# Kernel optimization log

Measured on AMD Instinct MI355X. Metric: run time of the kernel, lower is better.

Reference implementation:

```python
import jax, jax.numpy as jnp
import numpy as np

N_QUERY, N_BACKGND, DIM = 2048, 8192, 32


def setup_inputs() -> dict:
    key = jax.random.key(0)
    k0, k1, k2, k3 = jax.random.split(key, 4)
    x_backgnd = jax.random.normal(k0, (N_BACKGND, DIM), dtype=jnp.float32)
    y_backgnd = jax.random.normal(k1, (N_BACKGND,), dtype=jnp.float32)
    x_query = jax.random.normal(k2, (N_QUERY, DIM), dtype=jnp.float32)
    r = jax.random.uniform(k3, (N_QUERY, N_BACKGND), dtype=jnp.float32)
    sigma = jnp.array([0.1], dtype=jnp.float32)      # nn.Parameter init_sigma
    r_scale = jnp.array([3.0], dtype=jnp.float32)    # nn.Parameter init_r_scale
    w = jnp.ones((DIM,), dtype=jnp.float32)          # trainable weights matrix
    return {"x_backgnd": x_backgnd, "y_backgnd": y_backgnd, "x_query": x_query,
            "r": r, "sigma": sigma, "r_scale": r_scale, "w": w}


def reference(x_backgnd, y_backgnd, x_query, r, sigma, r_scale, w):
    # weighted Euclidean distance: ||(xq - xb) * w|| via the expansion trick,
    # avoiding the (n_query, n_backgnd, dim) difference tensor.
    xq = x_query * w           # (nq, d)
    xb = x_backgnd * w         # (nb, d)
    q2 = jnp.sum(xq * xq, axis=1, keepdims=True)        # (nq, 1)
    b2 = jnp.sum(xb * xb, axis=1)                        # (nb,)
    d2 = q2 + b2[None, :] - 2.0 * (xq @ xb.T)            # (nq, nb)
    dists = jnp.sqrt(jnp.maximum(d2, 0.0))
    # exp kernel with relationship bias, normalize, weighted sum
    k_vals = jnp.exp(-dists / sigma + r_scale * r)       # sigma, r_scale broadcast (1,)
    k_sum = jnp.sum(k_vals, axis=1, keepdims=True) + 1e-8
    weights = k_vals / k_sum
    y_pred = weights @ y_backgnd                          # (nq,)
    return y_pred
```

## Files before the change

kernel.cpp:

```cpp
#include <hip/hip_runtime.h>
#include <math.h>

#define NQ 2048
#define NB 8192
#define DIM 32

#define LOG2E 1.44269504088896340736f

typedef _Float16 half8 __attribute__((ext_vector_type(8)));
typedef float    f32x4 __attribute__((ext_vector_type(4)));

#define WS_ACC 0
#define WS_Q2  16448
#define WS_B2  24640
#define WS_XQH 57408
#define WS_XBH 188480

__global__ __launch_bounds__(256) void relnw_pre(
    const float* __restrict__ xq, const float* __restrict__ xb,
    const float* __restrict__ w,
    _Float16* __restrict__ XQh, _Float16* __restrict__ XBh,
    float* __restrict__ q2, float* __restrict__ b2,
    float* __restrict__ acc)
{
    const int tid = threadIdx.x;
    const int gi  = blockIdx.x * 256 + tid;
    if (gi < 2 * NQ) acc[gi] = 0.f;

    const int row = blockIdx.x * 64 + (tid >> 2);
    const int p   = tid & 3;
    if (row >= NQ + NB) return;

    const float* src; _Float16* dst; float* s2; float scale;
    if (row < NQ) { src = xq + (size_t)row * DIM;
                    dst = XQh + (size_t)row * DIM; s2 = q2 + row; scale = 1.f; }
    else          { int j = row - NQ;
                    src = xb + (size_t)j * DIM;
                    dst = XBh + (size_t)j * DIM;   s2 = b2 + j;   scale = -2.f; }

    const float4 xa  = ((const float4*)src)[p * 2];
    const float4 xbv = ((const float4*)src)[p * 2 + 1];
    const float4 wa  = ((const float4*)w)[p * 2];
    const float4 wb  = ((const float4*)w)[p * 2 + 1];
    const float xs[8]  = {xa.x, xa.y, xa.z, xa.w, xbv.x, xbv.y, xbv.z, xbv.w};
    const float ws_[8] = {wa.x, wa.y, wa.z, wa.w, wb.x, wb.y, wb.z, wb.w};

    half8 h;
    float s = 0.f;
#pragma unroll
    for (int c = 0; c < 8; ++c) {
        float t = xs[c] * ws_[c];
        _Float16 hh = (_Float16)t;
        float th = (float)hh;
        s = fmaf(th, th, s);
        h[c] = (_Float16)(th * scale);
    }
    *(half8*)(dst + p * 8) = h;

    s += __shfl_xor(s, 1, 64);
    s += __shfl_xor(s, 2, 64);
    if (p == 0) *s2 = s;
}

#define BT_PER_WAVE 16
#define BG_PER_WAVE (BT_PER_WAVE * 16)

#define GLDS(GSRC, LDST)                                                    \
  __builtin_amdgcn_global_load_lds(                                         \
      (const __attribute__((address_space(1))) void*)(GSRC),                \
      (__attribute__((address_space(3))) void*)(LDST), 16, 0, 0)

#define SBAR __builtin_amdgcn_sched_barrier(0)

#define COMPQ(BUF, QTR, AF)                                                 \
  { _Pragma("unroll") for (int it = 0; it < 4; ++it) {                      \
      const int co = (QTR) * 64 + it * 16 + quad * 4;                       \
      const f32x4 bb = *(const f32x4*)(b2l + co);                           \
      const f32x4 yv = *(const f32x4*)(ybl + co);                           \
      const f32x4 rr = *(const f32x4*)((BUF) + m * 256 +                    \
                           ((it * 64 + quad * 16) ^ swz));                  \
      f32x4 cin;                                                            \
      _Pragma("unroll") for (int g = 0; g < 4; ++g) cin[g] = q2s + bb[g];   \
      const f32x4 d2v = __builtin_amdgcn_mfma_f32_16x16x32_f16(             \
          AF[it], qfrag, cin, 0, 0, 0);                                     \
      _Pragma("unroll") for (int g = 0; g < 4; ++g) {                       \
        float d2   = fmaxf(d2v[g], 0.f);                                    \
        float dist = __builtin_amdgcn_sqrtf(d2);                            \
        float e    = fmaf(dist, c1, rr[g] * c2);                            \
        float k    = __builtin_amdgcn_exp2f(e);                             \
        sk += k;                                                            \
        sky = fmaf(k, yv[g], sky); } } }

__global__ __launch_bounds__(256, 2) void relnw_main(
    const _Float16* __restrict__ XQh,
    const _Float16* __restrict__ XBh,
    const float* __restrict__ q2,
    const float* __restrict__ b2,
    const float* __restrict__ yb,
    const float* __restrict__ r,
    const float* __restrict__ sigma,
    const float* __restrict__ rscale,
    float* __restrict__ acc)
{
    __shared__ char lds[4 * 8192 + 4 * 1024 + 4 * 1024];

    const int tid  = threadIdx.x;
    const int lane = tid & 63;
    const int wid  = tid >> 6;
    const int m    = lane & 15;
    const int quad = lane >> 4;

    const int q0     = blockIdx.y * 16;
    const int bstart = (blockIdx.x * 4 + wid) * BG_PER_WAVE;

    char*  bufA = lds + wid * 8192;
    char*  bufB = bufA + 4096;
    float* b2l  = (float*)(lds + 32768 + wid * 1024);
    float* ybl  = (float*)(lds + 36864 + wid * 1024);

    const float c1 = -LOG2E / sigma[0];
    const float c2 =  LOG2E * rscale[0];

    const half8 qfrag = *(const half8*)(XQh + (size_t)(q0 + m) * DIM + quad * 8);
    const float q2s   = q2[q0 + m];
    const int   swz   = (m & 7) << 4;

    const int g16 = lane >> 4;
    const int l16 = lane & 15;
    const char* rsrc[4];
#pragma unroll
    for (int j = 0; j < 4; ++j) {
        const int rw = 4 * j + g16;
        rsrc[j] = (const char*)(r + (size_t)(q0 + rw) * NB + bstart)
                  + ((l16 * 16) ^ ((rw & 7) << 4));
    }

#define AFRAG(I) (*(const half8*)(XBh + \
        (size_t)(bstart + (I) * 16 + m) * DIM + quad * 8))

    half8 afA[4], afB[4], afC[4], afD[4];
    float sk = 0.f, sky = 0.f;

#pragma unroll
    for (int i = 0; i < 4; ++i) afA[i] = AFRAG(i);
#pragma unroll
    for (int i = 0; i < 4; ++i) afB[i] = AFRAG(4 + i);
    GLDS((const char*)(b2 + bstart) + lane * 16, b2l);
    GLDS((const char*)(yb + bstart) + lane * 16, ybl);
#pragma unroll
    for (int j = 0; j < 4; ++j) GLDS(rsrc[j],       bufA + j * 1024);
#pragma unroll
    for (int j = 0; j < 4; ++j) GLDS(rsrc[j] + 256, bufB + j * 1024);
    SBAR;
    asm volatile("s_waitcnt vmcnt(4)" ::: "memory");
    SBAR;

    COMPQ(bufA, 0, afA)

#pragma unroll
    for (int i = 0; i < 4; ++i) afC[i] = AFRAG(8 + i);
#pragma unroll
    for (int i = 0; i < 4; ++i) afD[i] = AFRAG(12 + i);
#pragma unroll
    for (int j = 0; j < 4; ++j) GLDS(rsrc[j] + 512, bufA + j * 1024);
    SBAR;
    asm volatile("s_waitcnt vmcnt(12)" ::: "memory");
    SBAR;

    COMPQ(bufB, 1, afB)

#pragma unroll
    for (int j = 0; j < 4; ++j) GLDS(rsrc[j] + 768, bufB + j * 1024);
    SBAR;
    asm volatile("s_waitcnt vmcnt(4)" ::: "memory");
    SBAR;

    COMPQ(bufA, 2, afC)

    asm volatile("s_waitcnt vmcnt(0)" ::: "memory");
    SBAR;

    COMPQ(bufB, 3, afD)

    sk  += __shfl_xor(sk, 16, 64);
    sk  += __shfl_xor(sk, 32, 64);
    sky += __shfl_xor(sky, 16, 64);
    sky += __shfl_xor(sky, 32, 64);
    if (lane < 16) {
        atomicAdd(acc + (q0 + m),      sk);
        atomicAdd(acc + NQ + (q0 + m), sky);
    }
}

__global__ __launch_bounds__(256) void relnw_finalize(
    const float* __restrict__ acc, float* __restrict__ out)
{
    int q = blockIdx.x * 256 + threadIdx.x;
    if (q < NQ)
        out[q] = acc[NQ + q] / (acc[q] + 1e-8f);
}

extern "C" void kernel_launch(void* const* d_in, const int* in_sizes, int n_in,
                              void* d_out, int out_size, void* d_ws, size_t ws_size,
                              hipStream_t stream) {
    const float* xb     = (const float*)d_in[0];
    const float* yb     = (const float*)d_in[1];
    const float* xq     = (const float*)d_in[2];
    const float* r      = (const float*)d_in[3];
    const float* sigma  = (const float*)d_in[4];
    const float* rscale = (const float*)d_in[5];
    const float* w      = (const float*)d_in[6];
    float* out = (float*)d_out;

    char* ws = (char*)d_ws;
    float*    acc = (float*)(ws + WS_ACC);
    float*    q2  = (float*)(ws + WS_Q2);
    float*    b2  = (float*)(ws + WS_B2);
    _Float16* XQh = (_Float16*)(ws + WS_XQH);
    _Float16* XBh = (_Float16*)(ws + WS_XBH);

    relnw_pre<<<(NQ + NB) / 64, 256, 0, stream>>>(xq, xb, w, XQh, XBh, q2, b2, acc);

    dim3 grid(NB / (4 * BG_PER_WAVE), NQ / 16);
    relnw_main<<<grid, 256, 0, stream>>>(XQh, XBh, q2, b2, yb, r, sigma, rscale, acc);

    relnw_finalize<<<(NQ + 255) / 256, 256, 0, stream>>>(acc, out);
}
```

Before: 111.3 us.

## Share r tile loads across the block with wide per-row global-to-LDS copies

Each block now stages a shared 16x256 slice of r per quarter into LDS. Each wave loads 4 full rows with 1 KB contiguous per-row transfers, where before each wave loaded its own 256-column strips in 256-byte row segments. Waves then compute interleaved 64-column chunks from the shared buffer, which needs block-wide barriers between stages. The aim is longer contiguous DRAM bursts for the dominant r stream, at the cost of extra s_barrier synchronisation.

```diff
diff --git a/kernel.cpp b/kernel.cpp
--- a/kernel.cpp
+++ b/kernel.cpp
@@ -62,23 +62,25 @@
     if (p == 0) *s2 = s;
 }
 
-#define BT_PER_WAVE 16
-#define BG_PER_WAVE (BT_PER_WAVE * 16)
-
 #define GLDS(GSRC, LDST)                                                    \
   __builtin_amdgcn_global_load_lds(                                         \
       (const __attribute__((address_space(1))) void*)(GSRC),                \
       (__attribute__((address_space(3))) void*)(LDST), 16, 0, 0)
 
 #define SBAR __builtin_amdgcn_sched_barrier(0)
+#define BARRIER __builtin_amdgcn_s_barrier()
+
+#define STAGEQ(BUF, QTR)                                                    \
+  { _Pragma("unroll") for (int j_ = 0; j_ < 4; ++j_)                        \
+      GLDS(rq[j_] + (QTR) * 1024, (BUF) + (wid * 4 + j_) * 1024); }
 
 #define COMPQ(BUF, QTR, AF)                                                 \
   { _Pragma("unroll") for (int it = 0; it < 4; ++it) {                      \
-      const int co = (QTR) * 64 + it * 16 + quad * 4;                       \
+      const int co = (QTR) * 256 + wid * 64 + it * 16 + quad * 4;           \
       const f32x4 bb = *(const f32x4*)(b2l + co);                           \
       const f32x4 yv = *(const f32x4*)(ybl + co);                           \
-      const f32x4 rr = *(const f32x4*)((BUF) + m * 256 +                    \
-                           ((it * 64 + quad * 16) ^ swz));                  \
+      const f32x4 rr = *(const f32x4*)((BUF) + m * 1024 +                   \
+          ((wid * 256 + it * 64 + quad * 16) ^ swz));                       \
       f32x4 cin;                                                            \
       _Pragma("unroll") for (int g = 0; g < 4; ++g) cin[g] = q2s + bb[g];   \
       const f32x4 d2v = __builtin_amdgcn_mfma_f32_16x16x32_f16(             \
@@ -91,6 +93,9 @@
         sk += k;                                                            \
         sky = fmaf(k, yv[g], sky); } } }
 
+#define AFRAG(Q, I) (*(const half8*)(XBh +                                  \
+    (size_t)(bcol0 + (Q) * 256 + wid * 64 + (I) * 16 + m) * DIM + quad * 8))
+
 __global__ __launch_bounds__(256, 2) void relnw_main(
     const _Float16* __restrict__ XQh,
     const _Float16* __restrict__ XBh,
@@ -102,7 +107,7 @@
     const float* __restrict__ rscale,
     float* __restrict__ acc)
 {
-    __shared__ char lds[4 * 8192 + 4 * 1024 + 4 * 1024];
+    __shared__ char lds[2 * 16384 + 4096 + 4096];
 
     const int tid  = threadIdx.x;
     const int lane = tid & 63;
@@ -110,13 +115,13 @@
     const int m    = lane & 15;
     const int quad = lane >> 4;
 
-    const int q0     = blockIdx.y * 16;
-    const int bstart = (blockIdx.x * 4 + wid) * BG_PER_WAVE;
-
-    char*  bufA = lds + wid * 8192;
-    char*  bufB = bufA + 4096;
-    float* b2l  = (float*)(lds + 32768 + wid * 1024);
-    float* ybl  = (float*)(lds + 36864 + wid * 1024);
+    const int q0    = blockIdx.y * 16;
+    const int bcol0 = blockIdx.x * 1024;
+
+    char*  bufA = lds;
+    char*  bufB = lds + 16384;
+    float* b2l  = (float*)(lds + 32768);
+    float* ybl  = (float*)(lds + 36864);
 
     const float c1 = -LOG2E / sigma[0];
     const float c2 =  LOG2E * rscale[0];
@@ -125,62 +130,62 @@
     const float q2s   = q2[q0 + m];
     const int   swz   = (m & 7) << 4;
 
-    const int g16 = lane >> 4;
-    const int l16 = lane & 15;
-    const char* rsrc[4];
+    const char* rq[4];
 #pragma unroll
     for (int j = 0; j < 4; ++j) {
-        const int rw = 4 * j + g16;
-        rsrc[j] = (const char*)(r + (size_t)(q0 + rw) * NB + bstart)
-                  + ((l16 * 16) ^ ((rw & 7) << 4));
+        const int rw = wid * 4 + j;
+        rq[j] = (const char*)(r + (size_t)(q0 + rw) * NB + bcol0)
+                + ((lane * 16) ^ ((rw & 7) << 4));
     }
 
-#define AFRAG(I) (*(const half8*)(XBh + \
-        (size_t)(bstart + (I) * 16 + m) * DIM + quad * 8))
-
-    half8 afA[4], afB[4], afC[4], afD[4];
+    half8 af0[4], af1[4], af2[4], af3[4];
     float sk = 0.f, sky = 0.f;
 
 #pragma unroll
-    for (int i = 0; i < 4; ++i) afA[i] = AFRAG(i);
-#pragma unroll
-    for (int i = 0; i < 4; ++i) afB[i] = AFRAG(4 + i);
-    GLDS((const char*)(b2 + bstart) + lane * 16, b2l);
-    GLDS((const char*)(yb + bstart) + lane * 16, ybl);
-#pragma unroll
-    for (int j = 0; j < 4; ++j) GLDS(rsrc[j],       bufA + j * 1024);
-#pragma unroll
-    for (int j = 0; j < 4; ++j) GLDS(rsrc[j] + 256, bufB + j * 1024);
+    for (int i = 0; i < 4; ++i) af0[i] = AFRAG(0, i);
+#pragma unroll
+    for (int i = 0; i < 4; ++i) af1[i] = AFRAG(1, i);
+    GLDS((const char*)(b2 + bcol0) + wid * 1024 + (lane & 63) * 16,
+         (char*)b2l + wid * 1024);
+    GLDS((const char*)(yb + bcol0) + wid * 1024 + (lane & 63) * 16,
+         (char*)ybl + wid * 1024);
+    STAGEQ(bufA, 0)
+    STAGEQ(bufB, 1)
     SBAR;
     asm volatile("s_waitcnt vmcnt(4)" ::: "memory");
     SBAR;
-
-    COMPQ(bufA, 0, afA)
-
-#pragma unroll
-    for (int i = 0; i < 4; ++i) afC[i] = AFRAG(8 + i);
-#pragma unroll
-    for (int i = 0; i < 4; ++i) afD[i] = AFRAG(12 + i);
-#pragma unroll
-    for (int j = 0; j < 4; ++j) GLDS(rsrc[j] + 512, bufA + j * 1024);
+    BARRIER;
+
+    COMPQ(bufA, 0, af0)
+    BARRIER;
+
+#pragma unroll
+    for (int i = 0; i < 4; ++i) af2[i] = AFRAG(2, i);
+#pragma unroll
+    for (int i = 0; i < 4; ++i) af3[i] = AFRAG(3, i);
+    STAGEQ(bufA, 2)
     SBAR;
     asm volatile("s_waitcnt vmcnt(12)" ::: "memory");
     SBAR;
-
-    COMPQ(bufB, 1, afB)
-
-#pragma unroll
-    for (int j = 0; j < 4; ++j) GLDS(rsrc[j] + 768, bufB + j * 1024);
+    BARRIER;
+
+    COMPQ(bufB, 1, af1)
+    BARRIER;
+
+    STAGEQ(bufB, 3)
     SBAR;
     asm volatile("s_waitcnt vmcnt(4)" ::: "memory");
     SBAR;
-
-    COMPQ(bufA, 2, afC)
+    BARRIER;
+
+    COMPQ(bufA, 2, af2)
+    BARRIER;
 
     asm volatile("s_waitcnt vmcnt(0)" ::: "memory");
     SBAR;
-
-    COMPQ(bufB, 3, afD)
+    BARRIER;
+
+    COMPQ(bufB, 3, af3)
 
     sk  += __shfl_xor(sk, 16, 64);
     sk  += __shfl_xor(sk, 32, 64);
@@ -221,7 +226,7 @@
 
     relnw_pre<<<(NQ + NB) / 64, 256, 0, stream>>>(xq, xb, w, XQh, XBh, q2, b2, acc);
 
-    dim3 grid(NB / (4 * BG_PER_WAVE), NQ / 16);
+    dim3 grid(NB / 1024, NQ / 16);
     relnw_main<<<grid, 256, 0, stream>>>(XQh, XBh, q2, b2, yb, r, sigma, rscale, acc);
 
     relnw_finalize<<<(NQ + 255) / 256, 256, 0, stream>>>(acc, out);
```

New measurement: 110.0 us. Within noise of the previous version (-1.2%).
